# Kernel tuning notes

Hardware: AMD Instinct MI355X
Metric: run time of the kernel (lower is better)

The kernel has to match this reference:

```python
import jax, jax.numpy as jnp
import numpy as np

B, C, W, H = 16, 256, 32, 32  # L = W*H = 1024
NUM_HEAD = 4
DIM_HEAD = C  # dim_head defaults to in_channels


def setup_inputs() -> dict:
    key = jax.random.key(0)
    ks = jax.random.split(key, 6)
    s = 0.02  # small init scale, like trained linear weights
    return {
        "x": jax.random.normal(ks[0], (B, C, W, H), dtype=jnp.float32),
        "Wq": jax.random.normal(ks[1], (NUM_HEAD, DIM_HEAD, C), dtype=jnp.float32) * s,
        "Wk": jax.random.normal(ks[2], (NUM_HEAD, DIM_HEAD, C), dtype=jnp.float32) * s,
        "Wv": jax.random.normal(ks[3], (NUM_HEAD, DIM_HEAD, C), dtype=jnp.float32) * s,
        "Wo_w": jax.random.normal(ks[4], (C, NUM_HEAD * DIM_HEAD), dtype=jnp.float32) * s,
        "Wo_b": jax.random.normal(ks[5], (C,), dtype=jnp.float32) * s,
    }


def reference(x, Wq, Wk, Wv, Wo_w, Wo_b):
    b, c, w, h = x.shape
    L = w * h
    # [b,c,w,h] -> [b,L,c]
    xs = jnp.transpose(x, (0, 2, 3, 1)).reshape(b, L, c)
    # per-head projections (torch Linear: y = x @ W^T), batched over heads
    Q = jnp.einsum('blc,hdc->bhld', xs, Wq)
    K = jnp.einsum('blc,hdc->bhld', xs, Wk)
    V = jnp.einsum('blc,hdc->bhld', xs, Wv)
    # no softmax: scores = Q K^T, heads = scores V
    scores = jnp.einsum('bhld,bhmd->bhlm', Q, K)  # [b,H,L,L]
    heads = jnp.einsum('bhlm,bhmd->bhld', scores, V)  # [b,H,L,d]
    # concat heads along channel dim -> [b,L,H*d], then output projection
    cat = jnp.transpose(heads, (0, 2, 1, 3)).reshape(b, L, -1)
    z = cat @ Wo_w.T + Wo_b  # [b,L,c]
    return jnp.transpose(z, (0, 2, 1)).reshape(b, c, w, h)
```

## Files before the change

### kernel.cpp

```cpp
#include <hip/hip_runtime.h>
#include <hip/hip_bf16.h>

typedef __attribute__((ext_vector_type(8))) short s8v;
typedef __attribute__((ext_vector_type(4))) float f4v;

__device__ __forceinline__ ushort f2bf(float f) {
    __hip_bfloat16 h = __float2bfloat16(f);
    return __builtin_bit_cast(ushort, h);
}

__device__ __forceinline__ int fsw(int row) { return ((row >> 1) ^ (row >> 3)) & 3; }

__device__ __forceinline__ void gload16(const ushort* g, ushort* l) {
    __builtin_amdgcn_global_load_lds(
        (const __attribute__((address_space(1))) unsigned*)g,
        (__attribute__((address_space(3))) unsigned*)l, 16, 0, 0);
}

__device__ __forceinline__ void cvtw16(ushort* p, float4 a, float4 b) {
    s8v u;
    u[0] = (short)f2bf(a.x); u[1] = (short)f2bf(a.y);
    u[2] = (short)f2bf(a.z); u[3] = (short)f2bf(a.w);
    u[4] = (short)f2bf(b.x); u[5] = (short)f2bf(b.y);
    u[6] = (short)f2bf(b.z); u[7] = (short)f2bf(b.w);
    *(s8v*)p = u;
}

__device__ __forceinline__ void scatw(ushort* L, int c8, int d, float4 a, float4 b) {
    float v[8] = { a.x, a.y, a.z, a.w, b.x, b.y, b.z, b.w };
#pragma unroll
    for (int i = 0; i < 8; ++i) {
        int row = c8 + i;
        L[row * 32 + (((d >> 3) ^ fsw(row)) << 3) + (d & 7)] = f2bf(v[i]);
    }
}

template<int NT>
__device__ __forceinline__ void gemmS(
    const float* __restrict__ Xb, const float* __restrict__ Yb,
    ushort* lds, int row0, int col0, ushort* __restrict__ O, int ldo) {
    const int tid = threadIdx.x, wave = tid >> 6, lane = tid & 63;
    const int g = wave >> 2, w4 = wave & 3;
    const int wr = w4 >> 1, wc = w4 & 1;
    const int rA = lane & 15, kg = lane >> 4;
    const int tg = tid & 255;
    const int srow = tg >> 2, slot = tg & 3;
    const int kb = g * (NT * 32);
    ushort* LA = lds + g * 16384;
    ushort* LB = LA + 8192;
    const int wadr = srow * 32 + ((slot ^ fsw(srow)) << 3);
    const float* gx = Xb + (size_t)(row0 + srow) * 1024 + kb + slot * 8;
    const float* gy = Yb + (size_t)(col0 + srow) * 1024 + kb + slot * 8;
    f4v acc[2][2] = {};
    __syncthreads();

    float4 bx[4][2], by[4][2];
#pragma unroll
    for (int p = 0; p < 3; ++p) {
        bx[p][0] = *(const float4*)(gx + p * 32);
        bx[p][1] = *(const float4*)(gx + p * 32 + 4);
        by[p][0] = *(const float4*)(gy + p * 32);
        by[p][1] = *(const float4*)(gy + p * 32 + 4);
    }
    cvtw16(LA + wadr, bx[0][0], bx[0][1]);
    cvtw16(LB + wadr, by[0][0], by[0][1]);

#pragma unroll
    for (int t = 0; t < NT; ++t) {
        if (t + 3 < NT) {
            const int bi = (t + 3) & 3;
            bx[bi][0] = *(const float4*)(gx + (t + 3) * 32);
            bx[bi][1] = *(const float4*)(gx + (t + 3) * 32 + 4);
            by[bi][0] = *(const float4*)(gy + (t + 3) * 32);
            by[bi][1] = *(const float4*)(gy + (t + 3) * 32 + 4);
        }
        if (t + 1 < NT) {
            const int bi = (t + 1) & 3;
            cvtw16(LA + ((t + 1) & 3) * 2048 + wadr, bx[bi][0], bx[bi][1]);
            cvtw16(LB + ((t + 1) & 3) * 2048 + wadr, by[bi][0], by[bi][1]);
        }
        asm volatile("s_waitcnt lgkmcnt(0)" ::: "memory");
        __builtin_amdgcn_s_barrier();
        __builtin_amdgcn_sched_barrier(0);
        const ushort* pa = LA + (t & 3) * 2048;
        const ushort* pb = LB + (t & 3) * 2048;
        s8v a[2], b[2];
#pragma unroll
        for (int m = 0; m < 2; ++m) {
            int row = wr * 32 + m * 16 + rA;
            a[m] = *(const s8v*)&pa[row * 32 + ((kg ^ fsw(row)) << 3)];
        }
#pragma unroll
        for (int n = 0; n < 2; ++n) {
            int row = wc * 32 + n * 16 + rA;
            b[n] = *(const s8v*)&pb[row * 32 + ((kg ^ fsw(row)) << 3)];
        }
#pragma unroll
        for (int m = 0; m < 2; ++m)
#pragma unroll
            for (int n = 0; n < 2; ++n)
                acc[m][n] = __builtin_amdgcn_mfma_f32_16x16x32_bf16(a[m], b[n], acc[m][n], 0, 0, 0);
    }
    __syncthreads();
    float* red = (float*)lds;
    if (g == 1) {
#pragma unroll
        for (int m = 0; m < 2; ++m)
#pragma unroll
            for (int n = 0; n < 2; ++n)
                *(f4v*)&red[(w4 * 64 + lane) * 16 + (m * 2 + n) * 4] = acc[m][n];
    }
    __syncthreads();
    if (g == 0) {
        int r4 = (lane >> 4) * 4, cl = lane & 15;
#pragma unroll
        for (int m = 0; m < 2; ++m)
#pragma unroll
            for (int n = 0; n < 2; ++n) {
                f4v o = *(const f4v*)&red[(w4 * 64 + lane) * 16 + (m * 2 + n) * 4];
                f4v s = acc[m][n] + o;
                int row = row0 + wr * 32 + m * 16 + r4;
                int col = col0 + wc * 32 + n * 16 + cl;
#pragma unroll
                for (int r = 0; r < 4; ++r)
                    O[(size_t)(row + r) * ldo + col] = f2bf(s[r]);
            }
    }
}

template<int XT>
__device__ __forceinline__ void gemmWT(
    const float* __restrict__ Xw, const float* __restrict__ Yw,
    ushort* lds, int row0, int col0, ushort* __restrict__ O, int ldo) {
    const int NT = 4;
    const int tid = threadIdx.x, wave = tid >> 6, lane = tid & 63;
    const int g = wave >> 2, w4 = wave & 3;
    const int wr = w4 >> 1, wc = w4 & 1;
    const int rA = lane & 15, kg = lane >> 4;
    const int tg = tid & 255;
    const int kb = g * 128;
    ushort* LA = lds + g * 16384;
    ushort* LB = LA + 8192;
    const int dT = tg >> 3, c8 = (tg & 7) * 8;
    const int srow = tg >> 2, slot = tg & 3;
    const int wadr = srow * 32 + ((slot ^ fsw(srow)) << 3);
    f4v acc[2][2] = {};
    __syncthreads();

    float4 bx[4][2], by[4][2];
#pragma unroll
    for (int p = 0; p < 3; ++p) {
        if (XT) {
            bx[p][0] = *(const float4*)(Xw + (size_t)(kb + p * 32 + dT) * 256 + row0 + c8);
            bx[p][1] = *(const float4*)(Xw + (size_t)(kb + p * 32 + dT) * 256 + row0 + c8 + 4);
        } else {
            bx[p][0] = *(const float4*)(Xw + (size_t)(row0 + srow) * 1024 + kb + p * 32 + slot * 8);
            bx[p][1] = *(const float4*)(Xw + (size_t)(row0 + srow) * 1024 + kb + p * 32 + slot * 8 + 4);
        }
        by[p][0] = *(const float4*)(Yw + (size_t)(kb + p * 32 + dT) * 256 + col0 + c8);
        by[p][1] = *(const float4*)(Yw + (size_t)(kb + p * 32 + dT) * 256 + col0 + c8 + 4);
    }
    if (XT) scatw(LA, c8, dT, bx[0][0], bx[0][1]);
    else    cvtw16(LA + wadr, bx[0][0], bx[0][1]);
    scatw(LB, c8, dT, by[0][0], by[0][1]);

#pragma unroll
    for (int t = 0; t < NT; ++t) {
        if (t + 3 < NT) {
            const int bi = (t + 3) & 3;
            if (XT) {
                bx[bi][0] = *(const float4*)(Xw + (size_t)(kb + (t + 3) * 32 + dT) * 256 + row0 + c8);
                bx[bi][1] = *(const float4*)(Xw + (size_t)(kb + (t + 3) * 32 + dT) * 256 + row0 + c8 + 4);
            } else {
                bx[bi][0] = *(const float4*)(Xw + (size_t)(row0 + srow) * 1024 + kb + (t + 3) * 32 + slot * 8);
                bx[bi][1] = *(const float4*)(Xw + (size_t)(row0 + srow) * 1024 + kb + (t + 3) * 32 + slot * 8 + 4);
            }
            by[bi][0] = *(const float4*)(Yw + (size_t)(kb + (t + 3) * 32 + dT) * 256 + col0 + c8);
            by[bi][1] = *(const float4*)(Yw + (size_t)(kb + (t + 3) * 32 + dT) * 256 + col0 + c8 + 4);
        }
        if (t + 1 < NT) {
            const int bi = (t + 1) & 3;
            ushort* la = LA + ((t + 1) & 3) * 2048;
            ushort* lb = LB + ((t + 1) & 3) * 2048;
            if (XT) scatw(la, c8, dT, bx[bi][0], bx[bi][1]);
            else    cvtw16(la + wadr, bx[bi][0], bx[bi][1]);
            scatw(lb, c8, dT, by[bi][0], by[bi][1]);
        }
        asm volatile("s_waitcnt lgkmcnt(0)" ::: "memory");
        __builtin_amdgcn_s_barrier();
        __builtin_amdgcn_sched_barrier(0);
        const ushort* pa = LA + (t & 3) * 2048;
        const ushort* pb = LB + (t & 3) * 2048;
        s8v a[2], b[2];
#pragma unroll
        for (int m = 0; m < 2; ++m) {
            int row = wr * 32 + m * 16 + rA;
            a[m] = *(const s8v*)&pa[row * 32 + ((kg ^ fsw(row)) << 3)];
        }
#pragma unroll
        for (int n = 0; n < 2; ++n) {
            int row = wc * 32 + n * 16 + rA;
            b[n] = *(const s8v*)&pb[row * 32 + ((kg ^ fsw(row)) << 3)];
        }
#pragma unroll
        for (int m = 0; m < 2; ++m)
#pragma unroll
            for (int n = 0; n < 2; ++n)
                acc[m][n] = __builtin_amdgcn_mfma_f32_16x16x32_bf16(a[m], b[n], acc[m][n], 0, 0, 0);
    }
    __syncthreads();
    float* red = (float*)lds;
    if (g == 1) {
#pragma unroll
        for (int m = 0; m < 2; ++m)
#pragma unroll
            for (int n = 0; n < 2; ++n)
                *(f4v*)&red[(w4 * 64 + lane) * 16 + (m * 2 + n) * 4] = acc[m][n];
    }
    __syncthreads();
    if (g == 0) {
        int r4 = (lane >> 4) * 4, cl = lane & 15;
#pragma unroll
        for (int m = 0; m < 2; ++m)
#pragma unroll
            for (int n = 0; n < 2; ++n) {
                f4v o = *(const f4v*)&red[(w4 * 64 + lane) * 16 + (m * 2 + n) * 4];
                f4v s = acc[m][n] + o;
                int row = row0 + wr * 32 + m * 16 + r4;
                int col = col0 + wc * 32 + n * 16 + cl;
#pragma unroll
                for (int r = 0; r < 4; ++r)
                    O[(size_t)(row + r) * ldo + col] = f2bf(s[r]);
            }
    }
}

__device__ __forceinline__ void gemm64x8(
    const ushort* __restrict__ Xb, const ushort* __restrict__ Yb,
    int ldx, int ldy, ushort* lds, int row0, int col0, int K,
    ushort* __restrict__ O, int ldo) {
    const int tid = threadIdx.x, wave = tid >> 6, lane = tid & 63;
    const int g = wave >> 2, w4 = wave & 3;
    const int wr = w4 >> 1, wc = w4 & 1;
    const int rA = lane & 15, kg = lane >> 4;
    const int srow = w4 * 16 + (lane >> 2);
    const int scol = ((lane & 3) ^ fsw(srow)) * 8;
    const int K2 = K >> 1, NT = K2 >> 5, kb = g * K2;
    ushort* LA = lds + g * 16384;
    ushort* LB = LA + 8192;
    f4v acc[2][2] = {};
    __syncthreads();
    const ushort* gx = Xb + (size_t)(row0 + srow) * ldx + kb + scol;
    const ushort* gy = Yb + (size_t)(col0 + srow) * ldy + kb + scol;
    gload16(gx,      LA + w4 * 512);
    gload16(gy,      LB + w4 * 512);
    gload16(gx + 32, LA + 2048 + w4 * 512);
    gload16(gy + 32, LB + 2048 + w4 * 512);
    for (int t = 0; t < NT; ++t) {
        if (t + 2 < NT) {
            int s2 = (t + 2) & 3, kt = (t + 2) << 5;
            gload16(gx + kt, LA + s2 * 2048 + w4 * 512);
            gload16(gy + kt, LB + s2 * 2048 + w4 * 512);
            asm volatile("s_waitcnt vmcnt(4)" ::: "memory");
        } else if (t + 1 < NT) {
            asm volatile("s_waitcnt vmcnt(2)" ::: "memory");
        } else {
            asm volatile("s_waitcnt vmcnt(0)" ::: "memory");
        }
        __builtin_amdgcn_s_barrier();
        __builtin_amdgcn_sched_barrier(0);
        const ushort* pa = LA + (t & 3) * 2048;
        const ushort* pb = LB + (t & 3) * 2048;
        s8v a[2], b[2];
#pragma unroll
        for (int m = 0; m < 2; ++m) {
            int row = wr * 32 + m * 16 + rA;
            a[m] = *(const s8v*)&pa[row * 32 + ((kg ^ fsw(row)) << 3)];
        }
#pragma unroll
        for (int n = 0; n < 2; ++n) {
            int row = wc * 32 + n * 16 + rA;
            b[n] = *(const s8v*)&pb[row * 32 + ((kg ^ fsw(row)) << 3)];
        }
#pragma unroll
        for (int m = 0; m < 2; ++m)
#pragma unroll
            for (int n = 0; n < 2; ++n)
                acc[m][n] = __builtin_amdgcn_mfma_f32_16x16x32_bf16(a[m], b[n], acc[m][n], 0, 0, 0);
    }
    __syncthreads();
    float* red = (float*)lds;
    if (g == 1) {
#pragma unroll
        for (int m = 0; m < 2; ++m)
#pragma unroll
            for (int n = 0; n < 2; ++n)
                *(f4v*)&red[(w4 * 64 + lane) * 16 + (m * 2 + n) * 4] = acc[m][n];
    }
    __syncthreads();
    if (g == 0) {
        int r4 = (lane >> 4) * 4, cl = lane & 15;
#pragma unroll
        for (int m = 0; m < 2; ++m)
#pragma unroll
            for (int n = 0; n < 2; ++n) {
                f4v o = *(const f4v*)&red[(w4 * 64 + lane) * 16 + (m * 2 + n) * 4];
                f4v s = acc[m][n] + o;
                int row = row0 + wr * 32 + m * 16 + r4;
                int col = col0 + wc * 32 + n * 16 + cl;
#pragma unroll
                for (int r = 0; r < 4; ++r)
                    O[(size_t)(row + r) * ldo + col] = f2bf(s[r]);
            }
    }
}

__device__ __forceinline__ void gemm128x8(
    const ushort* __restrict__ Xb, const ushort* __restrict__ Yb,
    int ldx, int ldy, ushort* lds, int row0, int col0, int K,
    ushort* __restrict__ O, int ldo) {
    const int tid = threadIdx.x, wave = tid >> 6, lane = tid & 63;
    const int wr = wave >> 2, wc = wave & 3;
    const int rA = lane & 15, kg = lane >> 4;
    const int srow = wave * 16 + (lane >> 2);
    const int scol = ((lane & 3) ^ fsw(srow)) * 8;
    const int NT = K >> 5;
    ushort* LA = lds;
    ushort* LB = lds + 16384;
    f4v acc[4][2] = {};
    __syncthreads();
    const ushort* gx = Xb + (size_t)(row0 + srow) * ldx + scol;
    const ushort* gy = Yb + (size_t)(col0 + srow) * ldy + scol;
#pragma unroll
    for (int p = 0; p < 2; ++p) {
        gload16(gx + p * 32, LA + p * 4096 + wave * 512);
        gload16(gy + p * 32, LB + p * 4096 + wave * 512);
    }
    for (int t = 0; t < NT; ++t) {
        if (t + 2 < NT) {
            int s2 = (t + 2) & 3, kt = (t + 2) << 5;
            gload16(gx + kt, LA + s2 * 4096 + wave * 512);
            gload16(gy + kt, LB + s2 * 4096 + wave * 512);
            asm volatile("s_waitcnt vmcnt(4)" ::: "memory");
        } else if (t + 1 < NT) {
            asm volatile("s_waitcnt vmcnt(2)" ::: "memory");
        } else {
            asm volatile("s_waitcnt vmcnt(0)" ::: "memory");
        }
        __builtin_amdgcn_s_barrier();
        __builtin_amdgcn_sched_barrier(0);
        const ushort* pa = LA + (t & 3) * 4096;
        const ushort* pb = LB + (t & 3) * 4096;
        s8v a[4], b[2];
#pragma unroll
        for (int m = 0; m < 4; ++m) {
            int row = wr * 64 + m * 16 + rA;
            a[m] = *(const s8v*)&pa[row * 32 + ((kg ^ fsw(row)) << 3)];
        }
#pragma unroll
        for (int n = 0; n < 2; ++n) {
            int row = wc * 32 + n * 16 + rA;
            b[n] = *(const s8v*)&pb[row * 32 + ((kg ^ fsw(row)) << 3)];
        }
#pragma unroll
        for (int m = 0; m < 4; ++m)
#pragma unroll
            for (int n = 0; n < 2; ++n)
                acc[m][n] = __builtin_amdgcn_mfma_f32_16x16x32_bf16(a[m], b[n], acc[m][n], 0, 0, 0);
    }
    int r4 = (lane >> 4) * 4, cl = lane & 15;
#pragma unroll
    for (int m = 0; m < 4; ++m)
#pragma unroll
        for (int n = 0; n < 2; ++n) {
            int row = row0 + wr * 64 + m * 16 + r4;
            int col = col0 + wc * 32 + n * 16 + cl;
#pragma unroll
            for (int r = 0; r < 4; ++r)
                O[(size_t)(row + r) * ldo + col] = f2bf(acc[m][n][r]);
        }
}

__device__ __forceinline__ void gemmOUT(
    const ushort* __restrict__ Ga, const float* __restrict__ Xf,
    ushort* lds, int row0, int col0,
    float* __restrict__ O, const float* __restrict__ bias) {
    const int tid = threadIdx.x, wave = tid >> 6, lane = tid & 63;
    const int wr = wave >> 2, wc = wave & 3;
    const int rA = lane & 15, kg = lane >> 4;
    const int srowA = wave * 16 + (lane >> 2);
    const int scolA = ((lane & 3) ^ fsw(srowA)) * 8;
    ushort* LA = lds;
    ushort* LB = lds + 16384;
    const int kk = tid >> 4, l8 = (tid & 15) * 8;
    int wadr[8];
#pragma unroll
    for (int i = 0; i < 8; ++i) {
        int row = l8 + i;
        wadr[i] = row * 32 + (((kk >> 3) ^ fsw(row)) << 3) + (kk & 7);
    }
    const ushort* gA = Ga + (size_t)(row0 + srowA) * 256 + scolA;
    const float* gB = Xf + (size_t)kk * 1024 + col0 + l8;
    f4v acc[4][2] = {};
    __syncthreads();

    float4 ra[4], rb[4];
    gload16(gA + 0, LA + 0 * 4096 + wave * 512);
    ra[0] = *(const float4*)(gB);
    rb[0] = *(const float4*)(gB + 4);
    gload16(gA + 32, LA + 1 * 4096 + wave * 512);
    ra[1] = *(const float4*)(gB + 32768);
    rb[1] = *(const float4*)(gB + 32768 + 4);
    asm volatile("s_waitcnt vmcnt(0)" ::: "memory");
    {
        float v[8] = { ra[0].x, ra[0].y, ra[0].z, ra[0].w, rb[0].x, rb[0].y, rb[0].z, rb[0].w };
#pragma unroll
        for (int i = 0; i < 8; ++i) LB[wadr[i]] = f2bf(v[i]);
    }
    asm volatile("s_waitcnt lgkmcnt(0)" ::: "memory");
    __builtin_amdgcn_s_barrier();
    __builtin_amdgcn_sched_barrier(0);

#pragma unroll
    for (int t = 0; t < 8; ++t) {
        if (t + 1 < 8) {
            if (t + 2 < 8) {
                gload16(gA + (t + 2) * 32, LA + ((t + 2) & 3) * 4096 + wave * 512);
                ra[(t + 2) & 3] = *(const float4*)(gB + (size_t)(t + 2) * 32768);
                rb[(t + 2) & 3] = *(const float4*)(gB + (size_t)(t + 2) * 32768 + 4);
            }
            {
                const int bi = (t + 1) & 3;
                float v[8] = { ra[bi].x, ra[bi].y, ra[bi].z, ra[bi].w,
                               rb[bi].x, rb[bi].y, rb[bi].z, rb[bi].w };
                ushort* lb = LB + bi * 4096;
#pragma unroll
                for (int i = 0; i < 8; ++i) lb[wadr[i]] = f2bf(v[i]);
            }
            if (t + 2 < 8) { asm volatile("s_waitcnt vmcnt(3)" ::: "memory"); }
            else           { asm volatile("s_waitcnt vmcnt(0)" ::: "memory"); }
            asm volatile("s_waitcnt lgkmcnt(0)" ::: "memory");
            __builtin_amdgcn_s_barrier();
            __builtin_amdgcn_sched_barrier(0);
        }
        const ushort* pa = LA + (t & 3) * 4096;
        const ushort* pb = LB + (t & 3) * 4096;
        s8v a[4], b[2];
#pragma unroll
        for (int m = 0; m < 4; ++m) {
            int row = wr * 64 + m * 16 + rA;
            a[m] = *(const s8v*)&pa[row * 32 + ((kg ^ fsw(row)) << 3)];
        }
#pragma unroll
        for (int n = 0; n < 2; ++n) {
            int row = wc * 32 + n * 16 + rA;
            b[n] = *(const s8v*)&pb[row * 32 + ((kg ^ fsw(row)) << 3)];
        }
#pragma unroll
        for (int m = 0; m < 4; ++m)
#pragma unroll
            for (int n = 0; n < 2; ++n)
                acc[m][n] = __builtin_amdgcn_mfma_f32_16x16x32_bf16(a[m], b[n], acc[m][n], 0, 0, 0);
    }
    int r4 = (lane >> 4) * 4, cl = lane & 15;
#pragma unroll
    for (int m = 0; m < 4; ++m)
#pragma unroll
        for (int n = 0; n < 2; ++n) {
            int row = row0 + wr * 64 + m * 16 + r4;
            int col = col0 + wc * 32 + n * 16 + cl;
#pragma unroll
            for (int r = 0; r < 4; ++r)
                O[(size_t)(row + r) * 1024 + col] = acc[m][n][r] + bias[row + r];
        }
}

__global__ __launch_bounds__(512, 2) void kSP(
    const float* __restrict__ x, const float* __restrict__ Wq,
    const float* __restrict__ Wk, const float* __restrict__ Wv,
    const float* __restrict__ Wo,
    ushort* __restrict__ S16, ushort* __restrict__ A16, ushort* __restrict__ BT) {
    __shared__ __align__(16) ushort lds[32768];
    const int bid = blockIdx.x;
    int xcd = bid & 7, idx = bid >> 3;
    int b = 2 * xcd + (idx >> 4), t = idx & 15;
    const float* xb = x + (size_t)b * 262144;
    gemmS<16>(xb, xb, lds, (t >> 2) * 64, (t & 3) * 64, S16 + (size_t)b * 65536, 256);
    if (bid < 64) {
        int h = bid >> 4, t2 = bid & 15;
        gemmWT<1>(Wq + (size_t)h * 65536, Wk + (size_t)h * 65536, lds,
                  (t2 >> 2) * 64, (t2 & 3) * 64, A16 + (size_t)h * 65536, 256);
    } else if (bid < 128) {
        int q = bid - 64, h = q >> 4, t2 = q & 15;
        gemmWT<0>(Wo + (size_t)h * 256, Wv + (size_t)h * 65536, lds,
                  (t2 >> 2) * 64, (t2 & 3) * 64, BT + (size_t)h * 256, 1024);
    }
}

__global__ __launch_bounds__(512, 2) void kT1(
    const ushort* __restrict__ A16, const ushort* __restrict__ S16,
    ushort* __restrict__ T1) {
    __shared__ __align__(16) ushort lds[32768];
    int j = blockIdx.x, xcd = j & 7, idx = j >> 3;
    int b = 2 * xcd + (idx >> 4), h = (idx >> 2) & 3, tile = idx & 3;
    gemm128x8(A16 + (size_t)h * 65536, S16 + (size_t)b * 65536, 256, 256, lds,
              (tile >> 1) * 128, (tile & 1) * 128, 256,
              T1 + (size_t)b * 262144 + h * 256, 1024);
}

__global__ __launch_bounds__(512, 2) void kGT(
    const ushort* __restrict__ BT, const ushort* __restrict__ T1,
    ushort* __restrict__ GT) {
    __shared__ __align__(16) ushort lds[32768];
    int j = blockIdx.x, xcd = j & 7, idx = j >> 3;
    int b = 2 * xcd + (idx >> 4), tile = idx & 15;
    gemm64x8(BT, T1 + (size_t)b * 262144, 1024, 1024, lds,
             (tile >> 2) * 64, (tile & 3) * 64, 1024, GT + (size_t)b * 65536, 256);
}

__global__ __launch_bounds__(512, 2) void kOUT(
    const ushort* __restrict__ GT, const float* __restrict__ x,
    float* __restrict__ out, const float* __restrict__ bias) {
    __shared__ __align__(16) ushort lds[32768];
    int j = blockIdx.x, xcd = j & 7, idx = j >> 3;
    int b = 2 * xcd + (idx >> 4), tile = idx & 15;
    gemmOUT(GT + (size_t)b * 65536, x + (size_t)b * 262144, lds,
            (tile >> 3) * 128, (tile & 7) * 128, out + (size_t)b * 262144, bias);
}

extern "C" void kernel_launch(void* const* d_in, const int* in_sizes, int n_in,
                              void* d_out, int out_size, void* d_ws, size_t ws_size,
                              hipStream_t stream) {
    const float* x  = (const float*)d_in[0];
    const float* Wq = (const float*)d_in[1];
    const float* Wk = (const float*)d_in[2];
    const float* Wv = (const float*)d_in[3];
    const float* Wo = (const float*)d_in[4];
    const float* Wb = (const float*)d_in[5];

    char* ws = (char*)d_ws;
    ushort* T1  = (ushort*)(ws + 0);
    ushort* S16 = (ushort*)(ws + 16777216);
    ushort* GT  = (ushort*)(ws + 20971520);
    ushort* A16 = (ushort*)(ws + 25165824);
    ushort* BT  = (ushort*)(ws + 26214400);

    hipLaunchKernelGGL(kSP,  dim3(256), dim3(512), 0, stream,
                       x, Wq, Wk, Wv, Wo, S16, A16, BT);
    hipLaunchKernelGGL(kT1,  dim3(256), dim3(512), 0, stream, A16, S16, T1);
    hipLaunchKernelGGL(kGT,  dim3(256), dim3(512), 0, stream, BT, T1, GT);
    hipLaunchKernelGGL(kOUT, dim3(256), dim3(512), 0, stream, GT, x, (float*)d_out, Wb);
}
```

Measured before the change: 40.24 us.

## Exploit Gram symmetry in kSP and move BT weight fold into kT1

The per-batch Gram matrix X·Xᵀ is symmetric, so kSP now computes only the 10 upper-triangular 64x64 tiles per batch and mirror-writes the off-diagonal tiles transposed. This cuts that stage's block count from 256 to 160. The Wo·Wv fold (BT) moves from kSP into extra blocks of kT1, which makes kSP lighter while kT1 grows to 320 blocks. The mirrored stores are uncoalesced 8-byte writes, and the extra kT1 blocks lengthen that launch.

```diff
diff --git a/kernel.cpp b/kernel.cpp
--- a/kernel.cpp
+++ b/kernel.cpp
@@ -35,10 +35,10 @@
     }
 }
 
-template<int NT>
 __device__ __forceinline__ void gemmS(
-    const float* __restrict__ Xb, const float* __restrict__ Yb,
-    ushort* lds, int row0, int col0, ushort* __restrict__ O, int ldo) {
+    const float* __restrict__ Xb, ushort* lds, int row0, int col0,
+    ushort* __restrict__ S, int mirror) {
+    const int NT = 16;
     const int tid = threadIdx.x, wave = tid >> 6, lane = tid & 63;
     const int g = wave >> 2, w4 = wave & 3;
     const int wr = w4 >> 1, wc = w4 & 1;
@@ -50,7 +50,7 @@
     ushort* LB = LA + 8192;
     const int wadr = srow * 32 + ((slot ^ fsw(srow)) << 3);
     const float* gx = Xb + (size_t)(row0 + srow) * 1024 + kb + slot * 8;
-    const float* gy = Yb + (size_t)(col0 + srow) * 1024 + kb + slot * 8;
+    const float* gy = Xb + (size_t)(col0 + srow) * 1024 + kb + slot * 8;
     f4v acc[2][2] = {};
     __syncthreads();
 
@@ -121,9 +121,13 @@
                 f4v s = acc[m][n] + o;
                 int row = row0 + wr * 32 + m * 16 + r4;
                 int col = col0 + wc * 32 + n * 16 + cl;
-#pragma unroll
-                for (int r = 0; r < 4; ++r)
-                    O[(size_t)(row + r) * ldo + col] = f2bf(s[r]);
+                ushort4 tv = { f2bf(s[0]), f2bf(s[1]), f2bf(s[2]), f2bf(s[3]) };
+                S[(size_t)(row + 0) * 256 + col] = tv.x;
+                S[(size_t)(row + 1) * 256 + col] = tv.y;
+                S[(size_t)(row + 2) * 256 + col] = tv.z;
+                S[(size_t)(row + 3) * 256 + col] = tv.w;
+                if (mirror)
+                    *(ushort4*)&S[(size_t)col * 256 + row] = tv;
             }
     }
 }
@@ -477,35 +481,45 @@
 
 __global__ __launch_bounds__(512, 2) void kSP(
     const float* __restrict__ x, const float* __restrict__ Wq,
-    const float* __restrict__ Wk, const float* __restrict__ Wv,
-    const float* __restrict__ Wo,
-    ushort* __restrict__ S16, ushort* __restrict__ A16, ushort* __restrict__ BT) {
+    const float* __restrict__ Wk,
+    ushort* __restrict__ S16, ushort* __restrict__ A16) {
     __shared__ __align__(16) ushort lds[32768];
     const int bid = blockIdx.x;
-    int xcd = bid & 7, idx = bid >> 3;
-    int b = 2 * xcd + (idx >> 4), t = idx & 15;
-    const float* xb = x + (size_t)b * 262144;
-    gemmS<16>(xb, xb, lds, (t >> 2) * 64, (t & 3) * 64, S16 + (size_t)b * 65536, 256);
-    if (bid < 64) {
-        int h = bid >> 4, t2 = bid & 15;
+    if (bid < 160) {
+        int xcd = bid & 7, idx = bid >> 3;
+        int b = 2 * xcd + (idx >= 10);
+        int tri = (idx >= 10) ? idx - 10 : idx;
+        int ti, tj;
+        if (tri < 4)      { ti = 0; tj = tri; }
+        else if (tri < 7) { ti = 1; tj = tri - 3; }
+        else if (tri < 9) { ti = 2; tj = tri - 5; }
+        else              { ti = 3; tj = 3; }
+        const float* xb = x + (size_t)b * 262144;
+        gemmS(xb, lds, ti * 64, tj * 64, S16 + (size_t)b * 65536, ti != tj);
+    } else {
+        int q = bid - 160, h = q >> 4, t2 = q & 15;
         gemmWT<1>(Wq + (size_t)h * 65536, Wk + (size_t)h * 65536, lds,
                   (t2 >> 2) * 64, (t2 & 3) * 64, A16 + (size_t)h * 65536, 256);
-    } else if (bid < 128) {
-        int q = bid - 64, h = q >> 4, t2 = q & 15;
+    }
+}
+
+__global__ __launch_bounds__(512, 2) void kT1(
+    const ushort* __restrict__ A16, const ushort* __restrict__ S16,
+    const float* __restrict__ Wo, const float* __restrict__ Wv,
+    ushort* __restrict__ T1, ushort* __restrict__ BT) {
+    __shared__ __align__(16) ushort lds[32768];
+    int j = blockIdx.x;
+    if (j < 256) {
+        int xcd = j & 7, idx = j >> 3;
+        int b = 2 * xcd + (idx >> 4), h = (idx >> 2) & 3, tile = idx & 3;
+        gemm128x8(A16 + (size_t)h * 65536, S16 + (size_t)b * 65536, 256, 256, lds,
+                  (tile >> 1) * 128, (tile & 1) * 128, 256,
+                  T1 + (size_t)b * 262144 + h * 256, 1024);
+    } else {
+        int q = j - 256, h = q >> 4, t2 = q & 15;
         gemmWT<0>(Wo + (size_t)h * 256, Wv + (size_t)h * 65536, lds,
                   (t2 >> 2) * 64, (t2 & 3) * 64, BT + (size_t)h * 256, 1024);
     }
-}
-
-__global__ __launch_bounds__(512, 2) void kT1(
-    const ushort* __restrict__ A16, const ushort* __restrict__ S16,
-    ushort* __restrict__ T1) {
-    __shared__ __align__(16) ushort lds[32768];
-    int j = blockIdx.x, xcd = j & 7, idx = j >> 3;
-    int b = 2 * xcd + (idx >> 4), h = (idx >> 2) & 3, tile = idx & 3;
-    gemm128x8(A16 + (size_t)h * 65536, S16 + (size_t)b * 65536, 256, 256, lds,
-              (tile >> 1) * 128, (tile & 1) * 128, 256,
-              T1 + (size_t)b * 262144 + h * 256, 1024);
 }
 
 __global__ __launch_bounds__(512, 2) void kGT(
@@ -545,9 +559,8 @@
     ushort* A16 = (ushort*)(ws + 25165824);
     ushort* BT  = (ushort*)(ws + 26214400);
 
-    hipLaunchKernelGGL(kSP,  dim3(256), dim3(512), 0, stream,
-                       x, Wq, Wk, Wv, Wo, S16, A16, BT);
-    hipLaunchKernelGGL(kT1,  dim3(256), dim3(512), 0, stream, A16, S16, T1);
+    hipLaunchKernelGGL(kSP,  dim3(224), dim3(512), 0, stream, x, Wq, Wk, S16, A16);
+    hipLaunchKernelGGL(kT1,  dim3(320), dim3(512), 0, stream, A16, S16, Wo, Wv, T1, BT);
     hipLaunchKernelGGL(kGT,  dim3(256), dim3(512), 0, stream, BT, T1, GT);
     hipLaunchKernelGGL(kOUT, dim3(256), dim3(512), 0, stream, GT, x, (float*)d_out, Wb);
 }
```

Measured after the change: 39.72 us. No clear change (-1.3%).
